# Optimization experiments

Hardware: AMD Instinct MI355X
Metric: run time of the kernel (lower is better)

## Reference

```python
import math
import jax, jax.numpy as jnp
import numpy as np

HIDDEN_DIM = 256
NEG_INF = -1e30


def setup_inputs() -> dict:
    key = jax.random.key(0)
    k1, k2, k3, k4 = jax.random.split(key, 4)
    B, L_IN, L_MEM, D_IN, D_MEM = 16, 2048, 2048, 512, 512
    inputs = jax.random.normal(k1, (B, L_IN, D_IN), dtype=jnp.float32)
    memory = jax.random.normal(k2, (B, L_MEM, D_MEM), dtype=jnp.float32)
    memory_mask = jnp.ones((B, L_MEM), dtype=jnp.int32)
    W_in = jax.random.normal(k3, (D_IN, HIDDEN_DIM), dtype=jnp.float32) * (1.0 / math.sqrt(D_IN))
    W_mem = jax.random.normal(k4, (D_MEM, HIDDEN_DIM), dtype=jnp.float32) * (1.0 / math.sqrt(D_MEM))
    return {"inputs": inputs, "memory": memory, "memory_mask": memory_mask,
            "W_in": W_in, "W_mem": W_mem}


def reference(inputs, memory, memory_mask, W_in, W_mem):
    # Projections: Linear(bias=False) + ReLU (dropout is identity at drop_prob=0)
    inp_h = jax.nn.relu(jnp.einsum('bld,dh->blh', inputs, W_in))    # [B, L_in, H]
    mem_h = jax.nn.relu(jnp.einsum('bmd,dh->bmh', memory, W_mem))   # [B, L_mem, H]
    # Scaled dot-product scores
    scale = 1.0 / math.sqrt(HIDDEN_DIM)
    logits = jnp.einsum('blh,bmh->blm', inp_h, mem_h) * scale        # [B, L_in, L_mem]
    # Masked softmax over memory axis (mask broadcast over query axis)
    mask = (memory_mask > 0)[:, None, :]                             # [B, 1, L_mem]
    logits = jnp.where(mask, logits, NEG_INF)
    score = jax.nn.softmax(logits, axis=-1)                          # [B, L_in, L_mem]
    # Context over the ORIGINAL (unprojected) memory, then concat with inputs
    context = jnp.einsum('blm,bmd->bld', score, memory)              # [B, L_in, D_mem]
    return jnp.concatenate([context, inputs], axis=-1)               # [B, L_in, D_mem+D_in]
```

## Files before the change

kernel.cpp:

```cpp
#include <hip/hip_runtime.h>
#include <cstdint>
#include <cstddef>

typedef _Float16 f16;
typedef __attribute__((ext_vector_type(4)))  _Float16 f16x4;
typedef __attribute__((ext_vector_type(8)))  _Float16 f16x8;
typedef __attribute__((ext_vector_type(2)))  __fp16   fp16v2;
typedef __attribute__((ext_vector_type(4)))  float    f32x4;
typedef __attribute__((ext_vector_type(16))) float    f32x16;

static constexpr int BB = 16, LL = 2048, DIN = 512, HH = 256, DOUT = 1024;
static constexpr float SCALE = 0.0625f;
#define NEG_BIG (-1e30f)

__device__ __forceinline__ void gload16(const void* g, void* l) {
  __builtin_amdgcn_global_load_lds(
      (const __attribute__((address_space(1))) unsigned int*)g,
      (__attribute__((address_space(3))) unsigned int*)l, 16, 0, 0);
}

__device__ __forceinline__ unsigned pk2(float a, float b) {
  union { fp16v2 v; unsigned u; } c;
  c.v = __builtin_amdgcn_cvt_pkrtz(a, b);
  return c.u;
}

__global__ void wt2_kernel(const float* __restrict__ Wa, const float* __restrict__ Wb,
                           f16* __restrict__ WTa, f16* __restrict__ WTb) {
  int g = blockIdx.x * 256 + threadIdx.x;
  const float* W = (g < 131072) ? Wa : Wb;
  f16* WT = (g < 131072) ? WTa : WTb;
  int gg = g & 131071;
  int d = gg >> 8, h = gg & 255;
  WT[h * 512 + d] = (f16)W[gg];
}

__global__ void vt_kernel(const float* __restrict__ mem, f16* __restrict__ VT) {
  int m0 = blockIdx.x * 32, d0 = blockIdx.y * 32, b = blockIdx.z;
  __shared__ f16 t[32][36];
  int tid = threadIdx.x;
  {
    int r = tid >> 3, c4 = (tid & 7) * 4;
    float4 v = *(const float4*)(mem + (size_t)(b * LL + m0 + r) * DIN + d0 + c4);
    t[c4 + 0][r] = (f16)v.x; t[c4 + 1][r] = (f16)v.y;
    t[c4 + 2][r] = (f16)v.z; t[c4 + 3][r] = (f16)v.w;
  }
  __syncthreads();
  {
    int d = tid >> 3, seg = tid & 7;
    f16x4 hv = *(const f16x4*)&t[d][seg * 4];
    *(f16x4*)(VT + (size_t)(b * 512 + d0 + d) * 2048 + m0 + seg * 4) = hv;
  }
}

__global__ __launch_bounds__(256, 2) void proj_kernel(const float* __restrict__ Xa,
                                                      const float* __restrict__ Xb,
                                                      const f16* __restrict__ WTa,
                                                      const f16* __restrict__ WTb,
                                                      f16* __restrict__ Oa,
                                                      f16* __restrict__ Ob) {
  const float* X = blockIdx.z ? Xb : Xa;
  const f16* WT  = blockIdx.z ? WTb : WTa;
  f16* Out       = blockIdx.z ? Ob : Oa;
  const int Rbase = blockIdx.x * 128, Cbase = blockIdx.y * 128;
  __shared__ f16 a_t[128 * 40];
  __shared__ f16 b_t[128 * 32];
  const int tid = threadIdx.x, lane = tid & 63, wave = tid >> 6;
  const int wr = wave >> 1, wc = wave & 1;
  const int l15 = lane & 15, g4 = lane >> 4;
  f32x4 acc[4][4] = {};
  for (int ks = 0; ks < 16; ++ks) {
    __syncthreads();
#pragma unroll
    for (int k = 0; k < 4; ++k) {
      int idx = k * 256 + tid;
      int row = idx >> 3, c4 = idx & 7;
      float4 v = *(const float4*)(X + (size_t)(Rbase + row) * 512 + ks * 32 + c4 * 4);
      f16x4 hv = { (f16)v.x, (f16)v.y, (f16)v.z, (f16)v.w };
      *(f16x4*)((char*)a_t + row * 80 + c4 * 8) = hv;
    }
#pragma unroll
    for (int i = 0; i < 2; ++i) {
      int o = i * 4096 + wave * 1024 + lane * 16;
      int r = o >> 6, cp = o & 63;
      gload16((const char*)WT + (size_t)(Cbase + r) * 1024 + ks * 64 + (cp ^ ((r & 3) << 4)),
              (char*)b_t + i * 4096 + wave * 1024);
    }
    __syncthreads();
    f16x8 af[4], bf[4];
#pragma unroll
    for (int mi = 0; mi < 4; ++mi) {
      int r = wr * 64 + mi * 16 + l15;
      af[mi] = *(const f16x8*)((const char*)a_t + r * 80 + g4 * 16);
    }
#pragma unroll
    for (int ni = 0; ni < 4; ++ni) {
      int r = wc * 64 + ni * 16 + l15;
      bf[ni] = *(const f16x8*)((const char*)b_t + r * 64 + ((g4 * 16) ^ ((r & 3) << 4)));
    }
#pragma unroll
    for (int mi = 0; mi < 4; ++mi)
#pragma unroll
      for (int ni = 0; ni < 4; ++ni)
        acc[mi][ni] = __builtin_amdgcn_mfma_f32_16x16x32_f16(af[mi], bf[ni], acc[mi][ni], 0, 0, 0);
  }
#pragma unroll
  for (int mi = 0; mi < 4; ++mi)
#pragma unroll
    for (int ni = 0; ni < 4; ++ni)
#pragma unroll
      for (int di = 0; di < 4; ++di) {
        int row = Rbase + wr * 64 + mi * 16 + g4 * 4 + di;
        int col = Cbase + wc * 64 + ni * 16 + l15;
        float v = acc[mi][ni][di];
        Out[(size_t)row * 256 + col] = (f16)(v > 0.f ? v : 0.f);
      }
}

__global__ __launch_bounds__(512, 2) void attn_kernel(
    const float* __restrict__ X, const int* __restrict__ mask,
    const f16* __restrict__ Qh, const f16* __restrict__ Kh,
    const f16* __restrict__ VT, float* __restrict__ out) {
  const int bid = blockIdx.x;
  const int lb = ((bid & 7) << 5) | (bid >> 3);
  const int b = lb >> 4, qbase = (lb & 15) * 128;
  const int tid = threadIdx.x, lane = tid & 63, wave = tid >> 6;
  const int hi = lane >> 5, l31 = lane & 31;
  const int qsub = wave & 3, dvh = wave >> 2;
  __shared__ f16 KtBuf[2][32 * 256];
  __shared__ f16 VtBuf[2][512 * 32];
  __shared__ int Msk[2048];

#pragma unroll
  for (int k = 0; k < 32; ++k) {
    int f4 = k * 512 + tid;
    int row = f4 >> 7, c4 = f4 & 127;
    *(float4*)(out + (size_t)(b * LL + qbase + row) * DOUT + 512 + c4 * 4) =
        *(const float4*)(X + (size_t)(b * LL + qbase + row) * DIN + c4 * 4);
  }
  {
    int4 mv = *(const int4*)(mask + b * LL + tid * 4);
    *(int4*)&Msk[tid * 4] = mv;
  }

  const int qr = qbase + qsub * 32 + l31;
  f16x8 Qf[16];
  {
    const f16x8* qrow = (const f16x8*)(Qh + (size_t)(b * LL + qr) * HH);
#pragma unroll
    for (int c = 0; c < 16; ++c) Qf[c] = qrow[2 * c + hi];
  }
  f32x16 acc[8] = {};
  float m_run = NEG_BIG, l_run = 0.f;

  auto stage = [&](int bufi, int mbase) {
#pragma unroll
    for (int i = 0; i < 2; ++i) {
      int o = i * 8192 + wave * 1024 + lane * 16;
      int r = o >> 9, cp = o & 511;
      gload16((const char*)Kh + (size_t)(b * LL + mbase + r) * 512 + (cp ^ ((r & 31) << 4)),
              (char*)KtBuf[bufi] + i * 8192 + wave * 1024);
    }
#pragma unroll
    for (int i = 0; i < 4; ++i) {
      int o = i * 8192 + wave * 1024 + lane * 16;
      int dv = o >> 6, cp = o & 63;
      gload16((const char*)VT + (size_t)(b * 512 + dv) * 4096 + mbase * 2 + (cp ^ (((dv >> 1) & 3) << 4)),
              (char*)VtBuf[bufi] + i * 8192 + wave * 1024);
    }
  };

  stage(0, 0);
  __syncthreads();

  for (int mt = 0; mt < 64; ++mt) {
    const int cur = mt & 1;
    const int mbase = mt * 32;
    stage(cur ^ 1, ((mt + 1) & 63) * 32);
    asm volatile("s_waitcnt vmcnt(6)" ::: "memory");
    __builtin_amdgcn_sched_barrier(0);
    __builtin_amdgcn_s_barrier();

    const char* kb = (const char*)KtBuf[cur];
    const char* vb = (const char*)VtBuf[cur];

    f32x16 s0 = {}, s1 = {};
#pragma unroll
    for (int c = 0; c < 8; ++c) {
      f16x8 kf0 = *(const f16x8*)(kb + l31 * 512 + (((2 * c) * 32 + hi * 16) ^ (l31 << 4)));
      f16x8 kf1 = *(const f16x8*)(kb + l31 * 512 + (((2 * c + 1) * 32 + hi * 16) ^ (l31 << 4)));
      s0 = __builtin_amdgcn_mfma_f32_32x32x16_f16(kf0, Qf[2 * c], s0, 0, 0, 0);
      s1 = __builtin_amdgcn_mfma_f32_32x32x16_f16(kf1, Qf[2 * c + 1], s1, 0, 0, 0);
    }
    f32x16 s;
#pragma unroll
    for (int r = 0; r < 16; ++r) s[r] = s0[r] + s1[r];

    float tmax = NEG_BIG;
#pragma unroll
    for (int c2 = 0; c2 < 4; ++c2) {
      int4 mk = *(const int4*)&Msk[mbase + c2 * 8 + hi * 4];
      float x;
      x = s[4*c2+0] * SCALE; s[4*c2+0] = mk.x ? x : NEG_BIG;
      x = s[4*c2+1] * SCALE; s[4*c2+1] = mk.y ? x : NEG_BIG;
      x = s[4*c2+2] * SCALE; s[4*c2+2] = mk.z ? x : NEG_BIG;
      x = s[4*c2+3] * SCALE; s[4*c2+3] = mk.w ? x : NEG_BIG;
      tmax = fmaxf(tmax, fmaxf(fmaxf(s[4*c2+0], s[4*c2+1]), fmaxf(s[4*c2+2], s[4*c2+3])));
    }
    tmax = fmaxf(tmax, __shfl_xor(tmax, 32, 64));
    if (__any(tmax > m_run + 8.f)) {
      float mnew = fmaxf(m_run, tmax);
      float alpha = __expf(m_run - mnew);
      m_run = mnew;
      l_run *= alpha;
#pragma unroll
      for (int r = 0; r < 16; ++r) {
        float ar = __shfl(alpha, (r & 3) + 8 * (r >> 2) + 4 * hi, 32);
#pragma unroll
        for (int t = 0; t < 8; ++t) acc[t][r] *= ar;
      }
    }
    float tsum = 0.f;
#pragma unroll
    for (int r = 0; r < 16; ++r) {
      float e = __expf(s[r] - m_run);
      s[r] = e;
      tsum += e;
    }
    tsum += __shfl_xor(tsum, 32, 64);
    l_run += tsum;

    f16x8 pf[2];
#pragma unroll
    for (int j = 0; j < 2; ++j) {
      unsigned a0 = pk2(s[8*j+0], s[8*j+1]);
      unsigned a1 = pk2(s[8*j+2], s[8*j+3]);
      unsigned b0 = pk2(s[8*j+4], s[8*j+5]);
      unsigned b1 = pk2(s[8*j+6], s[8*j+7]);
      asm volatile("v_permlane32_swap_b32 %0, %1" : "+v"(a0), "+v"(b0));
      asm volatile("v_permlane32_swap_b32 %0, %1" : "+v"(a1), "+v"(b1));
      union { f16x8 v; unsigned u[4]; } un;
      un.u[0] = a0; un.u[1] = a1; un.u[2] = b0; un.u[3] = b1;
      pf[j] = un.v;
    }
#pragma unroll
    for (int j = 0; j < 2; ++j)
#pragma unroll
      for (int t = 0; t < 8; ++t) {
        int dvl = dvh * 256 + t * 32 + l31;
        f16x8 vf = *(const f16x8*)(vb + dvl * 64 + ((j * 32 + hi * 16) ^ (((dvl >> 1) & 3) << 4)));
        acc[t] = __builtin_amdgcn_mfma_f32_32x32x16_f16(pf[j], vf, acc[t], 0, 0, 0);
      }
    __builtin_amdgcn_s_barrier();
  }

  float linv = 1.f / l_run;
  float lr[16];
#pragma unroll
  for (int r = 0; r < 16; ++r) lr[r] = __shfl(linv, (r & 3) + 8 * (r >> 2) + 4 * hi, 32);
#pragma unroll
  for (int t = 0; t < 8; ++t) {
    int dv = dvh * 256 + t * 32 + l31;
#pragma unroll
    for (int r = 0; r < 16; ++r) {
      int q = qbase + qsub * 32 + (r & 3) + 8 * (r >> 2) + 4 * hi;
      out[(size_t)(b * LL + q) * DOUT + dv] = acc[t][r] * lr[r];
    }
  }
}

extern "C" void kernel_launch(void* const* d_in, const int* in_sizes, int n_in,
                              void* d_out, int out_size, void* d_ws, size_t ws_size,
                              hipStream_t stream) {
  const float* inputs = (const float*)d_in[0];
  const float* memory = (const float*)d_in[1];
  const int*   mmask  = (const int*)d_in[2];
  const float* W_in   = (const float*)d_in[3];
  const float* W_mem  = (const float*)d_in[4];
  float* out = (float*)d_out;

  char* ws = (char*)d_ws;
  f16* Qh  = (f16*)ws;
  f16* Kh  = (f16*)(ws + (16u << 20));
  f16* VT  = (f16*)(ws + (32u << 20));
  f16* WTi = (f16*)(ws + (64u << 20));
  f16* WTm = (f16*)(ws + (64u << 20) + (1u << 18));

  wt2_kernel<<<1024, 256, 0, stream>>>(W_in, W_mem, WTi, WTm);
  vt_kernel<<<dim3(64, 16, 16), 256, 0, stream>>>(memory, VT);
  proj_kernel<<<dim3(256, 2, 2), 256, 0, stream>>>(inputs, memory, WTi, WTm, Qh, Kh);
  attn_kernel<<<256, 512, 0, stream>>>(inputs, mmask, Qh, Kh, VT, out);
}
```

Baseline: 341.4 us.

## Software-pipeline QK and PV MFMAs across tiles with triple-buffered V

Restructures the attention loop so the QK^T MFMAs for the next memory tile are interleaved with the PV MFMAs of the previous tile, with softmax done after both. K stays double-buffered, V becomes triple-buffered, and two tiles are prefetched ahead. The aim is to hide softmax and LDS latency behind matrix work. The larger LDS footprint may reduce occupancy from two blocks per CU.

```diff
diff --git a/kernel.cpp b/kernel.cpp
--- a/kernel.cpp
+++ b/kernel.cpp
@@ -12,6 +12,9 @@
 static constexpr int BB = 16, LL = 2048, DIN = 512, HH = 256, DOUT = 1024;
 static constexpr float SCALE = 0.0625f;
 #define NEG_BIG (-1e30f)
+
+#define BAR()    __builtin_amdgcn_s_barrier()
+#define SCHED0() __builtin_amdgcn_sched_barrier(0)
 
 __device__ __forceinline__ void gload16(const void* g, void* l) {
   __builtin_amdgcn_global_load_lds(
@@ -128,7 +131,7 @@
   const int hi = lane >> 5, l31 = lane & 31;
   const int qsub = wave & 3, dvh = wave >> 2;
   __shared__ f16 KtBuf[2][32 * 256];
-  __shared__ f16 VtBuf[2][512 * 32];
+  __shared__ f16 VtBuf[3][512 * 32];
   __shared__ int Msk[2048];
 
 #pragma unroll
@@ -142,7 +145,6 @@
     int4 mv = *(const int4*)(mask + b * LL + tid * 4);
     *(int4*)&Msk[tid * 4] = mv;
   }
-
   const int qr = qbase + qsub * 32 + l31;
   f16x8 Qf[16];
   {
@@ -152,50 +154,31 @@
   }
   f32x16 acc[8] = {};
   float m_run = NEG_BIG, l_run = 0.f;
-
-  auto stage = [&](int bufi, int mbase) {
+  f16x8 pf[2];
+
+  auto stageK = [&](int bufi, int mbase) {
 #pragma unroll
     for (int i = 0; i < 2; ++i) {
       int o = i * 8192 + wave * 1024 + lane * 16;
       int r = o >> 9, cp = o & 511;
       gload16((const char*)Kh + (size_t)(b * LL + mbase + r) * 512 + (cp ^ ((r & 31) << 4)),
-              (char*)KtBuf[bufi] + i * 8192 + wave * 1024);
-    }
+              (char*)KtBuf[bufi] + o);
+    }
+  };
+  auto stageV = [&](int bufi, int mbase) {
 #pragma unroll
     for (int i = 0; i < 4; ++i) {
       int o = i * 8192 + wave * 1024 + lane * 16;
       int dv = o >> 6, cp = o & 63;
       gload16((const char*)VT + (size_t)(b * 512 + dv) * 4096 + mbase * 2 + (cp ^ (((dv >> 1) & 3) << 4)),
-              (char*)VtBuf[bufi] + i * 8192 + wave * 1024);
+              (char*)VtBuf[bufi] + o);
     }
   };
 
-  stage(0, 0);
-  __syncthreads();
-
-  for (int mt = 0; mt < 64; ++mt) {
-    const int cur = mt & 1;
-    const int mbase = mt * 32;
-    stage(cur ^ 1, ((mt + 1) & 63) * 32);
-    asm volatile("s_waitcnt vmcnt(6)" ::: "memory");
-    __builtin_amdgcn_sched_barrier(0);
-    __builtin_amdgcn_s_barrier();
-
-    const char* kb = (const char*)KtBuf[cur];
-    const char* vb = (const char*)VtBuf[cur];
-
-    f32x16 s0 = {}, s1 = {};
-#pragma unroll
-    for (int c = 0; c < 8; ++c) {
-      f16x8 kf0 = *(const f16x8*)(kb + l31 * 512 + (((2 * c) * 32 + hi * 16) ^ (l31 << 4)));
-      f16x8 kf1 = *(const f16x8*)(kb + l31 * 512 + (((2 * c + 1) * 32 + hi * 16) ^ (l31 << 4)));
-      s0 = __builtin_amdgcn_mfma_f32_32x32x16_f16(kf0, Qf[2 * c], s0, 0, 0, 0);
-      s1 = __builtin_amdgcn_mfma_f32_32x32x16_f16(kf1, Qf[2 * c + 1], s1, 0, 0, 0);
-    }
+  auto SM = [&](f32x16 s0, f32x16 s1, int mbase) {
     f32x16 s;
 #pragma unroll
     for (int r = 0; r < 16; ++r) s[r] = s0[r] + s1[r];
-
     float tmax = NEG_BIG;
 #pragma unroll
     for (int c2 = 0; c2 < 4; ++c2) {
@@ -229,8 +212,6 @@
     }
     tsum += __shfl_xor(tsum, 32, 64);
     l_run += tsum;
-
-    f16x8 pf[2];
 #pragma unroll
     for (int j = 0; j < 2; ++j) {
       unsigned a0 = pk2(s[8*j+0], s[8*j+1]);
@@ -243,15 +224,70 @@
       un.u[0] = a0; un.u[1] = a1; un.u[2] = b0; un.u[3] = b1;
       pf[j] = un.v;
     }
+  };
+
+  stageK(0, 0); stageK(1, 32);
+  stageV(0, 0); stageV(1, 32);
+  __syncthreads();
+  {
+    f32x16 s0 = {}, s1 = {};
+    const char* kb = (const char*)KtBuf[0];
+#pragma unroll
+    for (int c = 0; c < 8; ++c) {
+      f16x8 kf0 = *(const f16x8*)(kb + l31 * 512 + (((2 * c) * 32 + hi * 16) ^ (l31 << 4)));
+      f16x8 kf1 = *(const f16x8*)(kb + l31 * 512 + (((2 * c + 1) * 32 + hi * 16) ^ (l31 << 4)));
+      s0 = __builtin_amdgcn_mfma_f32_32x32x16_f16(kf0, Qf[2 * c], s0, 0, 0, 0);
+      s1 = __builtin_amdgcn_mfma_f32_32x32x16_f16(kf1, Qf[2 * c + 1], s1, 0, 0, 0);
+    }
+    SM(s0, s1, 0);
+  }
+
+  int vs = 0;
+  for (int t = 0; t < 63; ++t) {
+    BAR(); SCHED0();
+    stageK(t & 1, ((t + 2) & 63) * 32);
+    int vstage = vs + 2; if (vstage >= 3) vstage -= 3;
+    stageV(vstage, ((t + 2) & 63) * 32);
+    asm volatile("s_waitcnt vmcnt(6)" ::: "memory");
+    SCHED0(); BAR(); SCHED0();
+
+    const char* kb = (const char*)KtBuf[(t + 1) & 1];
+    const char* vb = (const char*)VtBuf[vs];
+    f32x16 s0 = {}, s1 = {};
+#pragma unroll
+    for (int c = 0; c < 8; ++c) {
+      f16x8 kf0 = *(const f16x8*)(kb + l31 * 512 + (((2 * c) * 32 + hi * 16) ^ (l31 << 4)));
+      f16x8 kf1 = *(const f16x8*)(kb + l31 * 512 + (((2 * c + 1) * 32 + hi * 16) ^ (l31 << 4)));
+      s0 = __builtin_amdgcn_mfma_f32_32x32x16_f16(kf0, Qf[2 * c], s0, 0, 0, 0);
+      s1 = __builtin_amdgcn_mfma_f32_32x32x16_f16(kf1, Qf[2 * c + 1], s1, 0, 0, 0);
+      int i0 = 2 * c, i1 = 2 * c + 1;
+      {
+        int j = i0 >> 3, tt = i0 & 7;
+        int dvl = dvh * 256 + tt * 32 + l31;
+        f16x8 vf = *(const f16x8*)(vb + dvl * 64 + ((j * 32 + hi * 16) ^ (((dvl >> 1) & 3) << 4)));
+        acc[tt] = __builtin_amdgcn_mfma_f32_32x32x16_f16(pf[j], vf, acc[tt], 0, 0, 0);
+      }
+      {
+        int j = i1 >> 3, tt = i1 & 7;
+        int dvl = dvh * 256 + tt * 32 + l31;
+        f16x8 vf = *(const f16x8*)(vb + dvl * 64 + ((j * 32 + hi * 16) ^ (((dvl >> 1) & 3) << 4)));
+        acc[tt] = __builtin_amdgcn_mfma_f32_32x32x16_f16(pf[j], vf, acc[tt], 0, 0, 0);
+      }
+    }
+    SM(s0, s1, (t + 1) * 32);
+    vs = vs + 1; if (vs == 3) vs = 0;
+  }
+
+  {
+    const char* vb = (const char*)VtBuf[vs];
 #pragma unroll
     for (int j = 0; j < 2; ++j)
 #pragma unroll
-      for (int t = 0; t < 8; ++t) {
-        int dvl = dvh * 256 + t * 32 + l31;
+      for (int tt = 0; tt < 8; ++tt) {
+        int dvl = dvh * 256 + tt * 32 + l31;
         f16x8 vf = *(const f16x8*)(vb + dvl * 64 + ((j * 32 + hi * 16) ^ (((dvl >> 1) & 3) << 4)));
-        acc[t] = __builtin_amdgcn_mfma_f32_32x32x16_f16(pf[j], vf, acc[t], 0, 0, 0);
-      }
-    __builtin_amdgcn_s_barrier();
+        acc[tt] = __builtin_amdgcn_mfma_f32_32x32x16_f16(pf[j], vf, acc[tt], 0, 0, 0);
+      }
   }
 
   float linv = 1.f / l_run;
```

Result: no change. 343.0 us (+0.4%).

## Split fused attention into QK/softmax-stats, stats reduce, and PV kernels

Applied to the files above, without the earlier changes.

Replaces the single flash-attention kernel with three kernels. The first computes per-tile QK scores, exponentiates them against a local tile max and stores the fp16 probabilities plus per-tile (max, sum) stats. The second reduces the stats to a global row max and inverse sum and copies the input half of the output. The third rescales each stored probability tile and multiplies it by V across a finer grid. The split is meant to raise parallelism and drop the online-rescale path, at the cost of writing and re-reading a 128MB score buffer and applying an fp16 rescale factor that may underflow.

```diff
diff --git a/kernel.cpp b/kernel.cpp
--- a/kernel.cpp
+++ b/kernel.cpp
@@ -11,7 +11,10 @@
 
 static constexpr int BB = 16, LL = 2048, DIN = 512, HH = 256, DOUT = 1024;
 static constexpr float SCALE = 0.0625f;
-#define NEG_BIG (-1e30f)
+#define MASKVAL (-30000.0f)
+
+#define BAR()    __builtin_amdgcn_s_barrier()
+#define SCHED0() __builtin_amdgcn_sched_barrier(0)
 
 __device__ __forceinline__ void gload16(const void* g, void* l) {
   __builtin_amdgcn_global_load_lds(
@@ -117,78 +120,40 @@
       }
 }
 
-__global__ __launch_bounds__(512, 2) void attn_kernel(
-    const float* __restrict__ X, const int* __restrict__ mask,
-    const f16* __restrict__ Qh, const f16* __restrict__ Kh,
-    const f16* __restrict__ VT, float* __restrict__ out) {
-  const int bid = blockIdx.x;
-  const int lb = ((bid & 7) << 5) | (bid >> 3);
-  const int b = lb >> 4, qbase = (lb & 15) * 128;
-  const int tid = threadIdx.x, lane = tid & 63, wave = tid >> 6;
+__global__ __launch_bounds__(64, 3) void sqk_kernel(
+    const int* __restrict__ mask, const f16* __restrict__ Qh, const f16* __restrict__ Kh,
+    f16* __restrict__ Sfrag, float2* __restrict__ Pstats) {
+  const int qtile = blockIdx.x, ms = blockIdx.y, b = blockIdx.z;
+  const int lane = threadIdx.x;
   const int hi = lane >> 5, l31 = lane & 31;
-  const int qsub = wave & 3, dvh = wave >> 2;
-  __shared__ f16 KtBuf[2][32 * 256];
-  __shared__ f16 VtBuf[2][512 * 32];
-  __shared__ int Msk[2048];
-
-#pragma unroll
-  for (int k = 0; k < 32; ++k) {
-    int f4 = k * 512 + tid;
-    int row = f4 >> 7, c4 = f4 & 127;
-    *(float4*)(out + (size_t)(b * LL + qbase + row) * DOUT + 512 + c4 * 4) =
-        *(const float4*)(X + (size_t)(b * LL + qbase + row) * DIN + c4 * 4);
-  }
-  {
-    int4 mv = *(const int4*)(mask + b * LL + tid * 4);
-    *(int4*)&Msk[tid * 4] = mv;
-  }
-
-  const int qr = qbase + qsub * 32 + l31;
+  __shared__ f16 Kt[32 * 256];
+
+  const int qg = qtile * 32 + l31;
   f16x8 Qf[16];
   {
-    const f16x8* qrow = (const f16x8*)(Qh + (size_t)(b * LL + qr) * HH);
+    const f16x8* qrow = (const f16x8*)(Qh + ((size_t)b * LL + qg) * HH);
 #pragma unroll
     for (int c = 0; c < 16; ++c) Qf[c] = qrow[2 * c + hi];
   }
-  f32x16 acc[8] = {};
-  float m_run = NEG_BIG, l_run = 0.f;
-
-  auto stage = [&](int bufi, int mbase) {
-#pragma unroll
-    for (int i = 0; i < 2; ++i) {
-      int o = i * 8192 + wave * 1024 + lane * 16;
+  const int* mrow = mask + b * LL;
+
+  for (int mt = ms * 16; mt < ms * 16 + 16; ++mt) {
+    const int mbase = mt * 32;
+#pragma unroll
+    for (int i = 0; i < 16; ++i) {
+      int o = i * 1024 + lane * 16;
       int r = o >> 9, cp = o & 511;
       gload16((const char*)Kh + (size_t)(b * LL + mbase + r) * 512 + (cp ^ ((r & 31) << 4)),
-              (char*)KtBuf[bufi] + i * 8192 + wave * 1024);
-    }
-#pragma unroll
-    for (int i = 0; i < 4; ++i) {
-      int o = i * 8192 + wave * 1024 + lane * 16;
-      int dv = o >> 6, cp = o & 63;
-      gload16((const char*)VT + (size_t)(b * 512 + dv) * 4096 + mbase * 2 + (cp ^ (((dv >> 1) & 3) << 4)),
-              (char*)VtBuf[bufi] + i * 8192 + wave * 1024);
-    }
-  };
-
-  stage(0, 0);
-  __syncthreads();
-
-  for (int mt = 0; mt < 64; ++mt) {
-    const int cur = mt & 1;
-    const int mbase = mt * 32;
-    stage(cur ^ 1, ((mt + 1) & 63) * 32);
-    asm volatile("s_waitcnt vmcnt(6)" ::: "memory");
-    __builtin_amdgcn_sched_barrier(0);
-    __builtin_amdgcn_s_barrier();
-
-    const char* kb = (const char*)KtBuf[cur];
-    const char* vb = (const char*)VtBuf[cur];
+              (char*)Kt + o);
+    }
+    asm volatile("s_waitcnt vmcnt(0)" ::: "memory");
+    SCHED0();
 
     f32x16 s0 = {}, s1 = {};
 #pragma unroll
     for (int c = 0; c < 8; ++c) {
-      f16x8 kf0 = *(const f16x8*)(kb + l31 * 512 + (((2 * c) * 32 + hi * 16) ^ (l31 << 4)));
-      f16x8 kf1 = *(const f16x8*)(kb + l31 * 512 + (((2 * c + 1) * 32 + hi * 16) ^ (l31 << 4)));
+      f16x8 kf0 = *(const f16x8*)((const char*)Kt + l31 * 512 + (((2 * c) * 32 + hi * 16) ^ (l31 << 4)));
+      f16x8 kf1 = *(const f16x8*)((const char*)Kt + l31 * 512 + (((2 * c + 1) * 32 + hi * 16) ^ (l31 << 4)));
       s0 = __builtin_amdgcn_mfma_f32_32x32x16_f16(kf0, Qf[2 * c], s0, 0, 0, 0);
       s1 = __builtin_amdgcn_mfma_f32_32x32x16_f16(kf1, Qf[2 * c + 1], s1, 0, 0, 0);
     }
@@ -196,39 +161,26 @@
 #pragma unroll
     for (int r = 0; r < 16; ++r) s[r] = s0[r] + s1[r];
 
-    float tmax = NEG_BIG;
+    float tmax = MASKVAL;
 #pragma unroll
     for (int c2 = 0; c2 < 4; ++c2) {
-      int4 mk = *(const int4*)&Msk[mbase + c2 * 8 + hi * 4];
+      int4 mk = *(const int4*)(mrow + mbase + c2 * 8 + hi * 4);
       float x;
-      x = s[4*c2+0] * SCALE; s[4*c2+0] = mk.x ? x : NEG_BIG;
-      x = s[4*c2+1] * SCALE; s[4*c2+1] = mk.y ? x : NEG_BIG;
-      x = s[4*c2+2] * SCALE; s[4*c2+2] = mk.z ? x : NEG_BIG;
-      x = s[4*c2+3] * SCALE; s[4*c2+3] = mk.w ? x : NEG_BIG;
+      x = s[4*c2+0] * SCALE; s[4*c2+0] = mk.x ? x : MASKVAL;
+      x = s[4*c2+1] * SCALE; s[4*c2+1] = mk.y ? x : MASKVAL;
+      x = s[4*c2+2] * SCALE; s[4*c2+2] = mk.z ? x : MASKVAL;
+      x = s[4*c2+3] * SCALE; s[4*c2+3] = mk.w ? x : MASKVAL;
       tmax = fmaxf(tmax, fmaxf(fmaxf(s[4*c2+0], s[4*c2+1]), fmaxf(s[4*c2+2], s[4*c2+3])));
     }
     tmax = fmaxf(tmax, __shfl_xor(tmax, 32, 64));
-    if (__any(tmax > m_run + 8.f)) {
-      float mnew = fmaxf(m_run, tmax);
-      float alpha = __expf(m_run - mnew);
-      m_run = mnew;
-      l_run *= alpha;
-#pragma unroll
-      for (int r = 0; r < 16; ++r) {
-        float ar = __shfl(alpha, (r & 3) + 8 * (r >> 2) + 4 * hi, 32);
-#pragma unroll
-        for (int t = 0; t < 8; ++t) acc[t][r] *= ar;
-      }
-    }
     float tsum = 0.f;
 #pragma unroll
     for (int r = 0; r < 16; ++r) {
-      float e = __expf(s[r] - m_run);
+      float e = __expf(s[r] - tmax);
       s[r] = e;
       tsum += e;
     }
     tsum += __shfl_xor(tsum, 32, 64);
-    l_run += tsum;
 
     f16x8 pf[2];
 #pragma unroll
@@ -243,28 +195,115 @@
       un.u[0] = a0; un.u[1] = a1; un.u[2] = b0; un.u[3] = b1;
       pf[j] = un.v;
     }
+    const size_t mtg = (size_t)b * 64 + mt;
 #pragma unroll
     for (int j = 0; j < 2; ++j)
-#pragma unroll
-      for (int t = 0; t < 8; ++t) {
-        int dvl = dvh * 256 + t * 32 + l31;
-        f16x8 vf = *(const f16x8*)(vb + dvl * 64 + ((j * 32 + hi * 16) ^ (((dvl >> 1) & 3) << 4)));
-        acc[t] = __builtin_amdgcn_mfma_f32_32x32x16_f16(pf[j], vf, acc[t], 0, 0, 0);
-      }
-    __builtin_amdgcn_s_barrier();
-  }
-
-  float linv = 1.f / l_run;
+      *(f16x8*)((char*)Sfrag + ((mtg * 2 + j) * 2048 + qg) * 32 + hi * 16) = pf[j];
+    if (hi == 0) {
+      float2 st; st.x = tmax; st.y = tsum;
+      Pstats[mtg * 2048 + qg] = st;
+    }
+  }
+}
+
+__global__ void stats_copy_kernel(const float* __restrict__ X, const float2* __restrict__ Pstats,
+                                  float* __restrict__ Mrow, float* __restrict__ Linv,
+                                  float* __restrict__ out) {
+  const int g = blockIdx.x, b = blockIdx.y;
+  const int tid = threadIdx.x;
+  const int row = g * 64 + (tid >> 2), sub = tid & 3;
+  float bm[16], bs[16];
+  float M = MASKVAL;
+#pragma unroll
+  for (int i = 0; i < 16; ++i) {
+    float2 p = Pstats[((size_t)b * 64 + sub * 16 + i) * 2048 + row];
+    bm[i] = p.x; bs[i] = p.y;
+    M = fmaxf(M, p.x);
+  }
+  M = fmaxf(M, __shfl_xor(M, 1, 64));
+  M = fmaxf(M, __shfl_xor(M, 2, 64));
+  float L = 0.f;
+#pragma unroll
+  for (int i = 0; i < 16; ++i) L += bs[i] * __expf(bm[i] - M);
+  L += __shfl_xor(L, 1, 64);
+  L += __shfl_xor(L, 2, 64);
+  if (sub == 0) {
+    Mrow[(size_t)b * 2048 + row] = M;
+    Linv[(size_t)b * 2048 + row] = 1.f / L;
+  }
+#pragma unroll
+  for (int it = 0; it < 32; ++it) {
+    int idx = it * 256 + tid;
+    int r = idx >> 7, c4 = idx & 127;
+    *(float4*)(out + ((size_t)b * 2048 + g * 64 + r) * 1024 + 512 + c4 * 4) =
+        *(const float4*)(X + ((size_t)b * 2048 + g * 64 + r) * 512 + c4 * 4);
+  }
+}
+
+__global__ __launch_bounds__(512, 4) void pv_kernel(
+    const f16* __restrict__ Sfrag, const float2* __restrict__ Pstats,
+    const float* __restrict__ Mrow, const float* __restrict__ Linv,
+    const f16* __restrict__ VT, float* __restrict__ out) {
+  const int qt = blockIdx.x, dt = blockIdx.y, b = blockIdx.z;
+  const int tid = threadIdx.x, lane = tid & 63, wave = tid >> 6;
+  const int hi = lane >> 5, l31 = lane & 31;
+  const int qs = wave & 3, dh = wave >> 2;
+  const int dvBase = dt * 128;
+  const int qg = qt * 128 + qs * 32 + l31;
+  __shared__ f16 Vt[2][128 * 32];
+
+  auto stage = [&](int bufi, int mt) {
+    int o = tid * 16;
+    int dv = o >> 6, cp = o & 63;
+    gload16((const char*)VT + (size_t)(b * 512 + dvBase + dv) * 4096 + mt * 64 + (cp ^ (((dv >> 1) & 3) << 4)),
+            (char*)Vt[bufi] + o);
+  };
+
+  const float Mq = Mrow[(size_t)b * 2048 + qg];
+  f32x16 acc[2] = {};
+
+  stage(0, 0);
+  __syncthreads();
+
+  for (int mt = 0; mt < 64; ++mt) {
+    const int cur = mt & 1;
+    stage(cur ^ 1, (mt + 1) & 63);
+    const size_t mtg = (size_t)b * 64 + mt;
+    float2 ps = Pstats[mtg * 2048 + qg];
+    f16x8 pf0 = *(const f16x8*)((const char*)Sfrag + ((mtg * 2 + 0) * 2048 + qg) * 32 + hi * 16);
+    f16x8 pf1 = *(const f16x8*)((const char*)Sfrag + ((mtg * 2 + 1) * 2048 + qg) * 32 + hi * 16);
+    asm volatile("s_waitcnt vmcnt(4)" ::: "memory");
+    SCHED0(); BAR(); SCHED0();
+
+    float fact = __expf(ps.x - Mq);
+    f16 fh = (f16)fact;
+    f16x8 fv = { fh, fh, fh, fh, fh, fh, fh, fh };
+    f16x8 pA0 = pf0 * fv;
+    f16x8 pA1 = pf1 * fv;
+
+    const char* vb = (const char*)Vt[cur];
+#pragma unroll
+    for (int dsub = 0; dsub < 2; ++dsub) {
+      int dvl = dh * 64 + dsub * 32 + l31;
+      f16x8 vf0 = *(const f16x8*)(vb + dvl * 64 + ((0 * 32 + hi * 16) ^ (((dvl >> 1) & 3) << 4)));
+      f16x8 vf1 = *(const f16x8*)(vb + dvl * 64 + ((1 * 32 + hi * 16) ^ (((dvl >> 1) & 3) << 4)));
+      acc[dsub] = __builtin_amdgcn_mfma_f32_32x32x16_f16(pA0, vf0, acc[dsub], 0, 0, 0);
+      acc[dsub] = __builtin_amdgcn_mfma_f32_32x32x16_f16(pA1, vf1, acc[dsub], 0, 0, 0);
+    }
+    BAR(); SCHED0();
+  }
+
+  float linv = Linv[(size_t)b * 2048 + qg];
   float lr[16];
 #pragma unroll
   for (int r = 0; r < 16; ++r) lr[r] = __shfl(linv, (r & 3) + 8 * (r >> 2) + 4 * hi, 32);
 #pragma unroll
-  for (int t = 0; t < 8; ++t) {
-    int dv = dvh * 256 + t * 32 + l31;
+  for (int dsub = 0; dsub < 2; ++dsub) {
+    int dv = dvBase + dh * 64 + dsub * 32 + l31;
 #pragma unroll
     for (int r = 0; r < 16; ++r) {
-      int q = qbase + qsub * 32 + (r & 3) + 8 * (r >> 2) + 4 * hi;
-      out[(size_t)(b * LL + q) * DOUT + dv] = acc[t][r] * lr[r];
+      int q = qt * 128 + qs * 32 + (r & 3) + 8 * (r >> 2) + 4 * hi;
+      out[((size_t)b * 2048 + q) * 1024 + dv] = acc[dsub][r] * lr[r];
     }
   }
 }
@@ -280,14 +319,20 @@
   float* out = (float*)d_out;
 
   char* ws = (char*)d_ws;
-  f16* Qh  = (f16*)ws;
-  f16* Kh  = (f16*)(ws + (16u << 20));
-  f16* VT  = (f16*)(ws + (32u << 20));
-  f16* WTi = (f16*)(ws + (64u << 20));
-  f16* WTm = (f16*)(ws + (64u << 20) + (1u << 18));
+  f16*    Qh     = (f16*)ws;
+  f16*    Kh     = (f16*)(ws + (16ull << 20));
+  f16*    VT     = (f16*)(ws + (32ull << 20));
+  f16*    WTi    = (f16*)(ws + (64ull << 20));
+  f16*    WTm    = (f16*)(ws + (64ull << 20) + (1u << 18));
+  f16*    Sfrag  = (f16*)(ws + (68ull << 20));
+  float2* Pstats = (float2*)(ws + (196ull << 20));
+  float*  MrowP  = (float*)(ws + (212ull << 20));
+  float*  LinvP  = (float*)(ws + (213ull << 20));
 
   wt2_kernel<<<1024, 256, 0, stream>>>(W_in, W_mem, WTi, WTm);
   vt_kernel<<<dim3(64, 16, 16), 256, 0, stream>>>(memory, VT);
   proj_kernel<<<dim3(256, 2, 2), 256, 0, stream>>>(inputs, memory, WTi, WTm, Qh, Kh);
-  attn_kernel<<<256, 512, 0, stream>>>(inputs, mmask, Qh, Kh, VT, out);
-}
+  sqk_kernel<<<dim3(64, 4, 16), 64, 0, stream>>>(mmask, Qh, Kh, Sfrag, Pstats);
+  stats_copy_kernel<<<dim3(32, 16), 256, 0, stream>>>(inputs, Pstats, MrowP, LinvP, out);
+  pv_kernel<<<dim3(16, 4, 16), 512, 0, stream>>>(Sfrag, Pstats, MrowP, LinvP, VT, out);
+}
```

New measurement: 369.1 us. 1.08x slower.
